# Kernel optimization log

Hardware: AMD Instinct MI355X
Metric: run time of the kernel (lower is better)

The kernel has to match this reference:

```python
import jax, jax.numpy as jnp
import numpy as np

N, B, OBS, ACT = 8, 32768, 128, 32
E, H = 128, 4
D = E // H  # attend_dim = 32
EPS = 1e-5


def setup_inputs() -> dict:
    key = jax.random.key(0)
    ks = jax.random.split(key, 20)
    sc = np.float32(0.02)
    inp = {
        "observation_vector": jax.random.normal(ks[0], (N, B, OBS), jnp.float32),
        "action_vector": jax.random.normal(ks[1], (N, B, ACT), jnp.float32),
        # per-agent BatchNorm affine params (training-mode batch stats are used)
        "bn_g_gamma": jnp.ones((N, OBS + ACT), jnp.float32),
        "bn_g_beta": jnp.zeros((N, OBS + ACT), jnp.float32),
        "bn_s_gamma": jnp.ones((N, OBS), jnp.float32),
        "bn_s_beta": jnp.zeros((N, OBS), jnp.float32),
        # per-agent g / state-only Linear layers
        "g_w": jax.random.normal(ks[2], (N, E, OBS + ACT), jnp.float32) * sc,
        "g_b": jnp.zeros((N, E), jnp.float32),
        "s_w": jax.random.normal(ks[3], (N, E, OBS), jnp.float32) * sc,
        "s_b": jnp.zeros((N, E), jnp.float32),
        # per-head attention projections (no bias)
        "wq": jax.random.normal(ks[4], (H, D, E), jnp.float32) * sc,
        "wk": jax.random.normal(ks[5], (H, D, E), jnp.float32) * sc,
        "wv": jax.random.normal(ks[6], (H, D, E), jnp.float32) * sc,
        # per-agent f networks: Linear(E + H*D -> E), Linear(E -> ACT)
        "f1_w": jax.random.normal(ks[7], (N, E, E + H * D), jnp.float32) * sc,
        "f1_b": jnp.zeros((N, E), jnp.float32),
        "f2_w": jax.random.normal(ks[8], (N, ACT, E), jnp.float32) * sc,
        "f2_b": jnp.zeros((N, ACT), jnp.float32),
    }
    return inp


def _bn(x, gamma, beta):
    # x: [N, B, F]; training-mode BatchNorm1d per agent (biased variance)
    mu = x.mean(axis=1, keepdims=True)
    var = x.var(axis=1, keepdims=True)
    return (x - mu) / jnp.sqrt(var + EPS) * gamma[:, None, :] + beta[:, None, :]


def _lrelu(x):
    return jax.nn.leaky_relu(x, 0.01)


def reference(observation_vector, action_vector, bn_g_gamma, bn_g_beta, bn_s_gamma,
              bn_s_beta, g_w, g_b, s_w, s_b, wq, wk, wv, f1_w, f1_b, f2_w, f2_b):
    obs, act = observation_vector, action_vector
    ga = jnp.concatenate([obs, act], axis=-1)                       # [N,B,OBS+ACT]
    e = _lrelu(jnp.einsum('nbf,nef->nbe', _bn(ga, bn_g_gamma, bn_g_beta), g_w)
               + g_b[:, None, :])                                   # [N,B,E]
    s = _lrelu(jnp.einsum('nbf,nef->nbe', _bn(obs, bn_s_gamma, bn_s_beta), s_w)
               + s_b[:, None, :])                                   # [N,B,E]
    q = jnp.einsum('nbe,hde->hnbd', e, wq)                          # [H,N,B,D]
    k = jnp.einsum('nbe,hde->hnbd', e, wk)
    v = _lrelu(jnp.einsum('nbe,hde->hnbd', e, wv))
    # leave-one-out attention over agents: mask the diagonal (self)
    logits = jnp.einsum('hnbd,hmbd->hbnm', q, k) / jnp.sqrt(jnp.float32(D))
    logits = jnp.where(jnp.eye(N, dtype=bool), -jnp.inf, logits)
    alpha = jax.nn.softmax(logits, axis=-1)                         # [H,B,N,N]
    xi = jnp.einsum('hbnm,hmbd->nbhd', alpha, v)                    # [N,B,H,D]
    xi = xi.reshape(N, xi.shape[1], H * D)
    fin = jnp.concatenate([xi, s], axis=-1)                         # [N,B,H*D+E]
    h1 = _lrelu(jnp.einsum('nbf,nef->nbe', fin, f1_w) + f1_b[:, None, :])
    all_q = jnp.einsum('nbe,nae->nba', h1, f2_w) + f2_b[:, None, :]  # [N,B,ACT]
    ids = jnp.argmax(act, axis=-1, keepdims=True)                   # [N,B,1]
    curr_q = jnp.take_along_axis(all_q, ids, axis=-1)               # [N,B,1]
    return curr_q
```

## Files before the change

kernel.cpp:

```cpp
#include <hip/hip_runtime.h>

#define N_AG 8
#define BTOT 32768
#define OBSF 128
#define ACTF 32
#define HH 4

#define WS_STATS   0u
#define WS_SCALES  (16u<<10)
#define WS_BIASES  (48u<<10)
#define WS_WQKV    (64u<<10)
#define WS_F2W     (160u<<10)
#define WS_F1W     (224u<<10)
#define WS_WG      (768u<<10)
#define WS_IDS     (1536u<<10)
#define WS_ES      (4u<<20)
#define WS_XI      (136u<<20)
#define WS_NEED    ((size_t)200<<20)

typedef __attribute__((ext_vector_type(8))) __bf16 bf16x8;
typedef __attribute__((ext_vector_type(8))) short short8;
typedef __attribute__((ext_vector_type(4))) float f32x4;

static __device__ __forceinline__ unsigned short f2bf(float f){
  unsigned u = __builtin_bit_cast(unsigned, f);
  u += 0x7fffu + ((u >> 16) & 1u);
  return (unsigned short)(u >> 16);
}
static __device__ __forceinline__ bf16x8 ldb8(const unsigned short* p){
  return __builtin_bit_cast(bf16x8, *(const short8*)p);
}
static __device__ __forceinline__ f32x4 mfma16(bf16x8 a, bf16x8 b, f32x4 c){
  return __builtin_amdgcn_mfma_f32_16x16x32_bf16(a, b, c, 0, 0, 0);
}

__global__ void k_zero(float* stats){
  for (int i = threadIdx.x; i < 2560; i += 256) stats[i] = 0.f;
}

__global__ __launch_bounds__(256) void k_stats_obs(const float* __restrict__ obs,
                                                   float* __restrict__ stats){
  int n = blockIdx.y, ch = blockIdx.x;
  int c = threadIdx.x & 31, r = threadIdx.x >> 5;
  const float4* p = (const float4*)(obs + ((size_t)n*BTOT + (size_t)ch*256 + r)*OBSF) + c;
  float sx=0.f, sy=0.f, sz=0.f, sw=0.f;
  float qx=0.f, qy=0.f, qz=0.f, qw=0.f;
  #pragma unroll 4
  for (int i = 0; i < 32; i++){
    float4 v = p[(size_t)i*8*(OBSF/4)];
    sx += v.x; sy += v.y; sz += v.z; sw += v.w;
    qx += v.x*v.x; qy += v.y*v.y; qz += v.z*v.z; qw += v.w*v.w;
  }
  __shared__ float4 rs[8][32], rq[8][32];
  rs[r][c] = make_float4(sx, sy, sz, sw);
  rq[r][c] = make_float4(qx, qy, qz, qw);
  __syncthreads();
  if (threadIdx.x < 128){
    int f = threadIdx.x;
    float ss = 0.f, qq = 0.f;
    #pragma unroll
    for (int g = 0; g < 8; g++){
      ss += ((const float*)&rs[g][f>>2])[f&3];
      qq += ((const float*)&rq[g][f>>2])[f&3];
    }
    atomicAdd(&stats[n*128 + f], ss);
    atomicAdd(&stats[1024 + n*128 + f], qq);
  }
}

__global__ __launch_bounds__(256) void k_stats_act(const float* __restrict__ act,
                                                   float* __restrict__ stats,
                                                   int* __restrict__ ids){
  int n = blockIdx.y, ch = blockIdx.x;
  int c = threadIdx.x & 7, r = threadIdx.x >> 3;
  int f0 = c*4;
  float sx=0.f, sy=0.f, sz=0.f, sw=0.f;
  float qx=0.f, qy=0.f, qz=0.f, qw=0.f;
  #pragma unroll
  for (int i = 0; i < 4; i++){
    int b = ch*128 + i*32 + r;
    float4 v = *(const float4*)(act + ((size_t)n*BTOT + b)*ACTF + f0);
    sx += v.x; sy += v.y; sz += v.z; sw += v.w;
    qx += v.x*v.x; qy += v.y*v.y; qz += v.z*v.z; qw += v.w*v.w;
    float mv = v.x; int mi = f0;
    if (v.y > mv){ mv = v.y; mi = f0+1; }
    if (v.z > mv){ mv = v.z; mi = f0+2; }
    if (v.w > mv){ mv = v.w; mi = f0+3; }
    #pragma unroll
    for (int m = 1; m <= 4; m <<= 1){
      float ov = __shfl_xor(mv, m);
      int   oi = __shfl_xor(mi, m);
      if (ov > mv || (ov == mv && oi < mi)){ mv = ov; mi = oi; }
    }
    if (c == 0) ids[(size_t)n*BTOT + b] = mi;
  }
  __shared__ float4 rs[32][8], rq[32][8];
  rs[r][c] = make_float4(sx, sy, sz, sw);
  rq[r][c] = make_float4(qx, qy, qz, qw);
  __syncthreads();
  if (threadIdx.x < 32){
    int f = threadIdx.x;
    float ss = 0.f, qq = 0.f;
    #pragma unroll
    for (int g = 0; g < 32; g++){
      ss += ((const float*)&rs[g][f>>2])[f&3];
      qq += ((const float*)&rq[g][f>>2])[f&3];
    }
    atomicAdd(&stats[2048 + n*32 + f], ss);
    atomicAdd(&stats[2304 + n*32 + f], qq);
  }
}

__global__ void k_finalize(const float* __restrict__ stats, const float* __restrict__ gg,
                           const float* __restrict__ gb, const float* __restrict__ sg,
                           const float* __restrict__ sb, float* __restrict__ scales){
  int n = blockIdx.x, f = threadIdx.x;
  if (f < 160){
    float mu, va;
    if (f < 128){ mu = stats[n*128+f] * (1.f/BTOT); va = stats[1024+n*128+f]*(1.f/BTOT) - mu*mu; }
    else { int fa = f-128; mu = stats[2048+n*32+fa]*(1.f/BTOT); va = stats[2304+n*32+fa]*(1.f/BTOT) - mu*mu; }
    float inv = 1.f / sqrtf(va + 1e-5f);
    float a = gg[n*160+f] * inv;
    scales[n*160+f] = a;
    scales[1280 + n*160+f] = gb[n*160+f] - mu*a;
    if (f < 128){
      float a2 = sg[n*128+f] * inv;
      scales[2560 + n*128+f] = a2;
      scales[3584 + n*128+f] = sb[n*128+f] - mu*a2;
    }
  }
}

__global__ void k_fold(const float* __restrict__ g_w, const float* __restrict__ g_b,
                       const float* __restrict__ s_w, const float* __restrict__ s_b,
                       const float* __restrict__ wq, const float* __restrict__ wk,
                       const float* __restrict__ wv, const float* __restrict__ f1w_in,
                       const float* __restrict__ f2w_in, const float* __restrict__ scales,
                       unsigned short* __restrict__ wg, float* __restrict__ bias_es,
                       unsigned short* __restrict__ wqkv, unsigned short* __restrict__ f1w,
                       unsigned short* __restrict__ f2w){
  int blk = blockIdx.x, t = threadIdx.x;
  if (blk < 2048){
    int n = blk >> 8, o = blk & 255;
    float part = 0.f;
    if (t < 160){
      float w, a, c;
      if (o < 128){ w = g_w[((size_t)n*128 + o)*160 + t]; a = scales[n*160+t]; c = scales[1280+n*160+t]; }
      else if (t < 128){ w = s_w[((size_t)n*128 + (o-128))*128 + t]; a = scales[2560+n*128+t]; c = scales[3584+n*128+t]; }
      else { w = 0.f; a = 0.f; c = 0.f; }
      wg[((size_t)n*256 + o)*160 + t] = f2bf(w*a);
      part = w * c;
    }
    __shared__ float red[256];
    red[t] = part; __syncthreads();
    for (int s2 = 128; s2 > 0; s2 >>= 1){ if (t < s2) red[t] += red[t+s2]; __syncthreads(); }
    if (t == 0){
      float base = (o < 128) ? g_b[n*128+o] : s_b[n*128+(o-128)];
      bias_es[n*256+o] = base + red[0];
    }
  } else if (blk < 2240){
    int idx = (blk-2048)*256 + t;
    int r = idx >> 7, f = idx & 127, rr = r & 127;
    const float* src = (r < 128) ? wq : (r < 256 ? wk : wv);
    wqkv[idx] = f2bf(src[rr*128 + f]);
  } else if (blk < 3264){
    int idx = (blk-2240)*256 + t;
    f1w[idx] = f2bf(f1w_in[idx]);
  } else {
    int idx = (blk-3264)*256 + t;
    f2w[idx] = f2bf(f2w_in[idx]);
  }
}

__global__ __launch_bounds__(256) void k_gemm_es(const float* __restrict__ obs,
    const float* __restrict__ act, const unsigned short* __restrict__ wg,
    const float* __restrict__ biases, unsigned short* __restrict__ es){
  int n = blockIdx.y, mbb = blockIdx.x;
  int tid = threadIdx.x, w = tid >> 6, l = tid & 63, lr = l & 15, lg = l >> 4;
  __shared__ unsigned short wsm[256*160];
  {
    const int4* src = (const int4*)(wg + (size_t)n*(256*160));
    int4* dst = (int4*)wsm;
    for (int i = tid; i < 256*160/8; i += 256) dst[i] = src[i];
  }
  int brow = mbb*128 + w*16 + lr;
  size_t bglob = (size_t)n*BTOT + brow;
  float4 x0[10];
  #pragma unroll
  for (int kt = 0; kt < 4; kt++){
    const float4* pa = (const float4*)(obs + bglob*OBSF + kt*32 + lg*8);
    x0[kt*2] = pa[0]; x0[kt*2+1] = pa[1];
  }
  { const float4* pa = (const float4*)(act + bglob*ACTF + lg*8);
    x0[8] = pa[0]; x0[9] = pa[1]; }
  __syncthreads();
  f32x4 zero = {0.f,0.f,0.f,0.f};
  bf16x8 af[5];
  #pragma unroll
  for (int kt = 0; kt < 5; kt++){
    float4 a = x0[kt*2], b = x0[kt*2+1];
    af[kt][0]=(__bf16)a.x; af[kt][1]=(__bf16)a.y; af[kt][2]=(__bf16)a.z; af[kt][3]=(__bf16)a.w;
    af[kt][4]=(__bf16)b.x; af[kt][5]=(__bf16)b.y; af[kt][6]=(__bf16)b.z; af[kt][7]=(__bf16)b.w;
  }
  float4 x1[10];
  #pragma unroll
  for (int kt = 0; kt < 4; kt++){
    const float4* pa = (const float4*)(obs + (bglob+64)*OBSF + kt*32 + lg*8);
    x1[kt*2] = pa[0]; x1[kt*2+1] = pa[1];
  }
  { const float4* pa = (const float4*)(act + (bglob+64)*ACTF + lg*8);
    x1[8] = pa[0]; x1[9] = pa[1]; }
  f32x4 acc[16];
  #pragma unroll
  for (int i = 0; i < 16; i++) acc[i] = zero;
  #pragma unroll
  for (int kt = 0; kt < 5; kt++)
    #pragma unroll
    for (int nt = 0; nt < 16; nt++){
      bf16x8 bf = ldb8(&wsm[(nt*16 + lr)*160 + kt*32 + lg*8]);
      acc[nt] = mfma16(af[kt], bf, acc[nt]);
    }
  #pragma unroll
  for (int nt = 0; nt < 16; nt++){
    int col = nt*16 + lr;
    float bias = biases[n*256 + col];
    #pragma unroll
    for (int r = 0; r < 4; r++){
      float v = acc[nt][r] + bias;
      v = v > 0.f ? v : 0.01f*v;
      int orow = mbb*128 + w*16 + lg*4 + r;
      es[((size_t)n*BTOT + orow)*256 + col] = f2bf(v);
    }
  }
  #pragma unroll
  for (int kt = 0; kt < 5; kt++){
    float4 a = x1[kt*2], b = x1[kt*2+1];
    af[kt][0]=(__bf16)a.x; af[kt][1]=(__bf16)a.y; af[kt][2]=(__bf16)a.z; af[kt][3]=(__bf16)a.w;
    af[kt][4]=(__bf16)b.x; af[kt][5]=(__bf16)b.y; af[kt][6]=(__bf16)b.z; af[kt][7]=(__bf16)b.w;
  }
  #pragma unroll
  for (int i = 0; i < 16; i++) acc[i] = zero;
  #pragma unroll
  for (int kt = 0; kt < 5; kt++)
    #pragma unroll
    for (int nt = 0; nt < 16; nt++){
      bf16x8 bf = ldb8(&wsm[(nt*16 + lr)*160 + kt*32 + lg*8]);
      acc[nt] = mfma16(af[kt], bf, acc[nt]);
    }
  #pragma unroll
  for (int nt = 0; nt < 16; nt++){
    int col = nt*16 + lr;
    float bias = biases[n*256 + col];
    #pragma unroll
    for (int r = 0; r < 4; r++){
      float v = acc[nt][r] + bias;
      v = v > 0.f ? v : 0.01f*v;
      int orow = mbb*128 + 64 + w*16 + lg*4 + r;
      es[((size_t)n*BTOT + orow)*256 + col] = f2bf(v);
    }
  }
}

__global__ __launch_bounds__(256) void k_attn(const unsigned short* __restrict__ es,
    const unsigned short* __restrict__ wqkv, unsigned short* __restrict__ xi){
  int bt = blockIdx.x;
  int tid = threadIdx.x, w = tid >> 6, l = tid & 63, lr = l & 15, lg = l >> 4;
  __shared__ unsigned short eT[128][136];
  __shared__ unsigned short qkvT[128][104];
  for (int i = tid; i < 128*16; i += 256){
    int row = i >> 4, c = (i & 15)*8;
    *(int4*)&eT[row][c] =
      *(const int4*)&es[((size_t)(row>>4)*BTOT + bt*16 + (row&15))*256 + c];
  }
  __syncthreads();
  for (int h = 0; h < HH; h++){
    f32x4 zero = {0.f,0.f,0.f,0.f};
    f32x4 acc[2][6];
    #pragma unroll
    for (int mt = 0; mt < 2; mt++)
      #pragma unroll
      for (int nt = 0; nt < 6; nt++) acc[mt][nt] = zero;
    #pragma unroll
    for (int kt = 0; kt < 4; kt++){
      int f0 = kt*32 + lg*8;
      bf16x8 a0 = ldb8(&eT[w*32 + lr][f0]);
      bf16x8 a1 = ldb8(&eT[w*32 + 16 + lr][f0]);
      #pragma unroll
      for (int nt = 0; nt < 6; nt++){
        int r = nt*16 + lr, sec = r >> 5, j = r & 31;
        bf16x8 bf = ldb8(&wqkv[((size_t)sec*128 + h*32 + j)*128 + f0]);
        acc[0][nt] = mfma16(a0, bf, acc[0][nt]);
        acc[1][nt] = mfma16(a1, bf, acc[1][nt]);
      }
    }
    __syncthreads();
    #pragma unroll
    for (int mt = 0; mt < 2; mt++)
      #pragma unroll
      for (int nt = 0; nt < 6; nt++)
        #pragma unroll
        for (int r = 0; r < 4; r++){
          float v = acc[mt][nt][r];
          if (nt >= 4) v = v > 0.f ? v : 0.01f*v;
          qkvT[w*32 + mt*16 + lg*4 + r][nt*16 + lr] = f2bf(v);
        }
    __syncthreads();
    {
      int dh = tid & 1, bi = (tid >> 1) & 15, nq = tid >> 5;
      int rq = nq*16 + bi;
      float qv[16];
      { bf16x8 t0 = ldb8(&qkvT[rq][dh*16]);
        bf16x8 t1 = ldb8(&qkvT[rq][dh*16 + 8]);
        #pragma unroll
        for (int i = 0; i < 8; i++){ qv[i] = (float)t0[i]; qv[8+i] = (float)t1[i]; } }
      float lgt[8];
      #pragma unroll
      for (int m = 0; m < 8; m++){
        bf16x8 k0 = ldb8(&qkvT[m*16+bi][32 + dh*16]);
        bf16x8 k1 = ldb8(&qkvT[m*16+bi][32 + dh*16 + 8]);
        float d = 0.f;
        #pragma unroll
        for (int i = 0; i < 8; i++){ d += qv[i]*(float)k0[i]; d += qv[8+i]*(float)k1[i]; }
        d += __shfl_xor(d, 1);
        lgt[m] = d * 0.17677669529663687f;
      }
      float mx = -1e30f;
      #pragma unroll
      for (int m = 0; m < 8; m++) if (m != nq) mx = fmaxf(mx, lgt[m]);
      float p[8], sum = 0.f;
      #pragma unroll
      for (int m = 0; m < 8; m++){ p[m] = (m == nq) ? 0.f : __expf(lgt[m] - mx); sum += p[m]; }
      float inv = 1.f / sum;
      float xa[16];
      #pragma unroll
      for (int i = 0; i < 16; i++) xa[i] = 0.f;
      #pragma unroll
      for (int m = 0; m < 8; m++){
        float al = p[m]*inv;
        bf16x8 v0 = ldb8(&qkvT[m*16+bi][64 + dh*16]);
        bf16x8 v1 = ldb8(&qkvT[m*16+bi][64 + dh*16 + 8]);
        #pragma unroll
        for (int i = 0; i < 8; i++){ xa[i] += al*(float)v0[i]; xa[8+i] += al*(float)v1[i]; }
      }
      short8 o0, o1;
      #pragma unroll
      for (int i = 0; i < 8; i++){ o0[i] = (short)f2bf(xa[i]); o1[i] = (short)f2bf(xa[8+i]); }
      size_t orow = (size_t)nq*BTOT + bt*16 + bi;
      *(short8*)&xi[orow*128 + h*32 + dh*16]     = o0;
      *(short8*)&xi[orow*128 + h*32 + dh*16 + 8] = o1;
    }
  }
}

__global__ __launch_bounds__(256) void k_gemm_f(const unsigned short* __restrict__ xi,
    const unsigned short* __restrict__ es, const unsigned short* __restrict__ f1w,
    const float* __restrict__ f1b, const unsigned short* __restrict__ f2w,
    const float* __restrict__ f2b, const int* __restrict__ ids,
    float* __restrict__ out){
  int n = blockIdx.y, mbb = blockIdx.x;
  int tid = threadIdx.x, w = tid >> 6, l = tid & 63, lr = l & 15, lg = l >> 4;
  __shared__ unsigned short f1T[128*264];
  __shared__ unsigned short f2T[32*136];
  __shared__ unsigned short h1T[64*136];
  __shared__ float allq[64*32];
  for (int i = tid; i < 128*32; i += 256){
    int r = i >> 5, c = (i & 31)*8;
    *(int4*)&f1T[r*264 + c] = *(const int4*)&f1w[((size_t)n*128 + r)*256 + c];
  }
  for (int i = tid; i < 32*16; i += 256){
    int r = i >> 4, c = (i & 15)*8;
    *(int4*)&f2T[r*136 + c] = *(const int4*)&f2w[((size_t)n*32 + r)*128 + c];
  }
  bf16x8 xf[2][8];
  {
    int arow0 = mbb*256 + w*16 + lr;
    #pragma unroll
    for (int kt = 0; kt < 4; kt++)
      xf[0][kt] = ldb8(&xi[((size_t)n*BTOT + arow0)*128 + kt*32 + lg*8]);
    #pragma unroll
    for (int kt = 0; kt < 4; kt++)
      xf[0][4+kt] = ldb8(&es[((size_t)n*BTOT + arow0)*256 + 128 + kt*32 + lg*8]);
  }
  __syncthreads();
  f32x4 zero = {0.f,0.f,0.f,0.f};
  #pragma unroll
  for (int sub = 0; sub < 4; sub++){
    const int cur = sub & 1, nxt = cur ^ 1;
    int mb = mbb*4 + sub;
    if (sub < 3){
      int arown = mb*64 + 64 + w*16 + lr;
      #pragma unroll
      for (int kt = 0; kt < 4; kt++)
        xf[nxt][kt] = ldb8(&xi[((size_t)n*BTOT + arown)*128 + kt*32 + lg*8]);
      #pragma unroll
      for (int kt = 0; kt < 4; kt++)
        xf[nxt][4+kt] = ldb8(&es[((size_t)n*BTOT + arown)*256 + 128 + kt*32 + lg*8]);
    }
    f32x4 a1[8];
    #pragma unroll
    for (int i = 0; i < 8; i++) a1[i] = zero;
    #pragma unroll
    for (int kt = 0; kt < 8; kt++)
      #pragma unroll
      for (int nt = 0; nt < 8; nt++){
        bf16x8 bf = ldb8(&f1T[(nt*16 + lr)*264 + kt*32 + lg*8]);
        a1[nt] = mfma16(xf[cur][kt], bf, a1[nt]);
      }
    #pragma unroll
    for (int nt = 0; nt < 8; nt++){
      int col = nt*16 + lr;
      float bias = f1b[n*128 + col];
      #pragma unroll
      for (int r = 0; r < 4; r++){
        float v = a1[nt][r] + bias;
        v = v > 0.f ? v : 0.01f*v;
        h1T[(w*16 + lg*4 + r)*136 + col] = f2bf(v);
      }
    }
    __syncthreads();
    f32x4 a2[2];
    a2[0] = zero; a2[1] = zero;
    #pragma unroll
    for (int kt = 0; kt < 4; kt++){
      int f0 = kt*32 + lg*8;
      bf16x8 hf = ldb8(&h1T[(w*16 + lr)*136 + f0]);
      #pragma unroll
      for (int nt = 0; nt < 2; nt++){
        bf16x8 bf = ldb8(&f2T[(nt*16 + lr)*136 + f0]);
        a2[nt] = mfma16(hf, bf, a2[nt]);
      }
    }
    #pragma unroll
    for (int nt = 0; nt < 2; nt++){
      int col = nt*16 + lr;
      float bias = f2b[n*32 + col];
      #pragma unroll
      for (int r = 0; r < 4; r++)
        allq[(w*16 + lg*4 + r)*32 + col] = a2[nt][r] + bias;
    }
    __syncthreads();
    if (tid < 64){
      size_t bglob = (size_t)mb*64 + tid;
      int id = ids[(size_t)n*BTOT + bglob];
      out[(size_t)n*BTOT + bglob] = allq[tid*32 + id];
    }
  }
}

extern "C" void kernel_launch(void* const* d_in, const int* in_sizes, int n_in,
                              void* d_out, int out_size, void* d_ws, size_t ws_size,
                              hipStream_t stream){
  if (ws_size < WS_NEED) return;
  const float* obs  = (const float*)d_in[0];
  const float* act  = (const float*)d_in[1];
  const float* gg   = (const float*)d_in[2];
  const float* gb   = (const float*)d_in[3];
  const float* sg   = (const float*)d_in[4];
  const float* sb   = (const float*)d_in[5];
  const float* g_w  = (const float*)d_in[6];
  const float* g_b  = (const float*)d_in[7];
  const float* s_w  = (const float*)d_in[8];
  const float* s_b  = (const float*)d_in[9];
  const float* wq   = (const float*)d_in[10];
  const float* wk   = (const float*)d_in[11];
  const float* wv   = (const float*)d_in[12];
  const float* f1w_in = (const float*)d_in[13];
  const float* f1b  = (const float*)d_in[14];
  const float* f2w_in = (const float*)d_in[15];
  const float* f2b  = (const float*)d_in[16];
  char* ws = (char*)d_ws;
  float* stats   = (float*)(ws + WS_STATS);
  float* scales  = (float*)(ws + WS_SCALES);
  float* bias_es = (float*)(ws + WS_BIASES);
  unsigned short* wqkv = (unsigned short*)(ws + WS_WQKV);
  unsigned short* f2wb = (unsigned short*)(ws + WS_F2W);
  unsigned short* f1wb = (unsigned short*)(ws + WS_F1W);
  unsigned short* wg   = (unsigned short*)(ws + WS_WG);
  int* ids             = (int*)(ws + WS_IDS);
  unsigned short* esb  = (unsigned short*)(ws + WS_ES);
  unsigned short* xib  = (unsigned short*)(ws + WS_XI);
  float* out = (float*)d_out;

  k_zero<<<1, 256, 0, stream>>>(stats);
  k_stats_obs<<<dim3(128,8), 256, 0, stream>>>(obs, stats);
  k_stats_act<<<dim3(256,8), 256, 0, stream>>>(act, stats, ids);
  k_finalize<<<8, 256, 0, stream>>>(stats, gg, gb, sg, sb, scales);
  k_fold<<<3392, 256, 0, stream>>>(g_w, g_b, s_w, s_b, wq, wk, wv, f1w_in, f2w_in,
                                   scales, wg, bias_es, wqkv, f1wb, f2wb);
  k_gemm_es<<<dim3(256,8), 256, 0, stream>>>(obs, act, wg, bias_es, esb);
  k_attn<<<2048, 256, 0, stream>>>(esb, wqkv, xib);
  k_gemm_f<<<dim3(128,8), 256, 0, stream>>>(xib, esb, f1wb, f1b, f2wb, f2b, ids, out);
}
```

Baseline: 374.0 us.

## Keep attention input fragments in registers and double-buffer QKV shared tile

The attention kernel now loads its E rows straight from global memory into register fragments instead of staging them through a shared eT tile. The QKV staging buffer is double-buffered by head parity, which removes one of the two barriers per head, and the head loop is unrolled. A launch bound of 3 blocks is added to raise occupancy. The trade is higher register pressure, and since eT was larger than the second qkvT buffer, the kernel also uses less shared memory.

```diff
diff --git a/kernel.cpp b/kernel.cpp
--- a/kernel.cpp
+++ b/kernel.cpp
@@ -261,19 +261,25 @@
   }
 }
 
-__global__ __launch_bounds__(256) void k_attn(const unsigned short* __restrict__ es,
+__global__ __launch_bounds__(256, 3) void k_attn(const unsigned short* __restrict__ es,
     const unsigned short* __restrict__ wqkv, unsigned short* __restrict__ xi){
   int bt = blockIdx.x;
   int tid = threadIdx.x, w = tid >> 6, l = tid & 63, lr = l & 15, lg = l >> 4;
-  __shared__ unsigned short eT[128][136];
-  __shared__ unsigned short qkvT[128][104];
-  for (int i = tid; i < 128*16; i += 256){
-    int row = i >> 4, c = (i & 15)*8;
-    *(int4*)&eT[row][c] =
-      *(const int4*)&es[((size_t)(row>>4)*BTOT + bt*16 + (row&15))*256 + c];
-  }
-  __syncthreads();
+  __shared__ unsigned short qkvT[2][128][104];
+  bf16x8 e0[4], e1[4];
+  {
+    int r0 = w*32 + lr, r1 = r0 + 16;
+    const unsigned short* p0 = &es[((size_t)(r0>>4)*BTOT + bt*16 + (r0&15))*256];
+    const unsigned short* p1 = &es[((size_t)(r1>>4)*BTOT + bt*16 + (r1&15))*256];
+    #pragma unroll
+    for (int kt = 0; kt < 4; kt++){
+      e0[kt] = ldb8(p0 + kt*32 + lg*8);
+      e1[kt] = ldb8(p1 + kt*32 + lg*8);
+    }
+  }
+  #pragma unroll
   for (int h = 0; h < HH; h++){
+    const int hb = h & 1;
     f32x4 zero = {0.f,0.f,0.f,0.f};
     f32x4 acc[2][6];
     #pragma unroll
@@ -283,17 +289,14 @@
     #pragma unroll
     for (int kt = 0; kt < 4; kt++){
       int f0 = kt*32 + lg*8;
-      bf16x8 a0 = ldb8(&eT[w*32 + lr][f0]);
-      bf16x8 a1 = ldb8(&eT[w*32 + 16 + lr][f0]);
       #pragma unroll
       for (int nt = 0; nt < 6; nt++){
         int r = nt*16 + lr, sec = r >> 5, j = r & 31;
         bf16x8 bf = ldb8(&wqkv[((size_t)sec*128 + h*32 + j)*128 + f0]);
-        acc[0][nt] = mfma16(a0, bf, acc[0][nt]);
-        acc[1][nt] = mfma16(a1, bf, acc[1][nt]);
-      }
-    }
-    __syncthreads();
+        acc[0][nt] = mfma16(e0[kt], bf, acc[0][nt]);
+        acc[1][nt] = mfma16(e1[kt], bf, acc[1][nt]);
+      }
+    }
     #pragma unroll
     for (int mt = 0; mt < 2; mt++)
       #pragma unroll
@@ -302,22 +305,22 @@
         for (int r = 0; r < 4; r++){
           float v = acc[mt][nt][r];
           if (nt >= 4) v = v > 0.f ? v : 0.01f*v;
-          qkvT[w*32 + mt*16 + lg*4 + r][nt*16 + lr] = f2bf(v);
+          qkvT[hb][w*32 + mt*16 + lg*4 + r][nt*16 + lr] = f2bf(v);
         }
     __syncthreads();
     {
       int dh = tid & 1, bi = (tid >> 1) & 15, nq = tid >> 5;
       int rq = nq*16 + bi;
       float qv[16];
-      { bf16x8 t0 = ldb8(&qkvT[rq][dh*16]);
-        bf16x8 t1 = ldb8(&qkvT[rq][dh*16 + 8]);
+      { bf16x8 t0 = ldb8(&qkvT[hb][rq][dh*16]);
+        bf16x8 t1 = ldb8(&qkvT[hb][rq][dh*16 + 8]);
         #pragma unroll
         for (int i = 0; i < 8; i++){ qv[i] = (float)t0[i]; qv[8+i] = (float)t1[i]; } }
       float lgt[8];
       #pragma unroll
       for (int m = 0; m < 8; m++){
-        bf16x8 k0 = ldb8(&qkvT[m*16+bi][32 + dh*16]);
-        bf16x8 k1 = ldb8(&qkvT[m*16+bi][32 + dh*16 + 8]);
+        bf16x8 k0 = ldb8(&qkvT[hb][m*16+bi][32 + dh*16]);
+        bf16x8 k1 = ldb8(&qkvT[hb][m*16+bi][32 + dh*16 + 8]);
         float d = 0.f;
         #pragma unroll
         for (int i = 0; i < 8; i++){ d += qv[i]*(float)k0[i]; d += qv[8+i]*(float)k1[i]; }
@@ -337,8 +340,8 @@
       #pragma unroll
       for (int m = 0; m < 8; m++){
         float al = p[m]*inv;
-        bf16x8 v0 = ldb8(&qkvT[m*16+bi][64 + dh*16]);
-        bf16x8 v1 = ldb8(&qkvT[m*16+bi][64 + dh*16 + 8]);
+        bf16x8 v0 = ldb8(&qkvT[hb][m*16+bi][64 + dh*16]);
+        bf16x8 v1 = ldb8(&qkvT[hb][m*16+bi][64 + dh*16 + 8]);
         #pragma unroll
         for (int i = 0; i < 8; i++){ xa[i] += al*(float)v0[i]; xa[8+i] += al*(float)v1[i]; }
       }
```

Measured after the change: 343.6 us. -8.1%, faster.
